# Performance work log

Measured on AMD Instinct MI355X. Metric: run time of the kernel, lower is better.

The kernel has to match this reference:

```python
import jax, jax.numpy as jnp
import numpy as np

EMBED_DIM = 1024
NUM_HEADS = 16
HEAD_DIM = EMBED_DIM // NUM_HEADS
ROPE_BASE = 10000.0


def _rope_cos_sin(seq_len, head_dim, dtype=jnp.float32):
    inv_freq = 1.0 / (ROPE_BASE ** (jnp.arange(0, head_dim, 2, dtype=jnp.float32) / head_dim))
    t = jnp.arange(seq_len, dtype=jnp.float32)
    freqs = jnp.outer(t, inv_freq)            # [N, D/2]
    emb = jnp.concatenate([freqs, freqs], -1)  # [N, D]
    return jnp.cos(emb).astype(dtype), jnp.sin(emb).astype(dtype)


def _rotate_half(x):
    x1, x2 = jnp.split(x, 2, axis=-1)
    return jnp.concatenate([-x2, x1], axis=-1)


def setup_inputs() -> dict:
    key = jax.random.key(0)
    k1, k2, k3 = jax.random.split(key, 3)
    B, N, C = 2, 2048, EMBED_DIM
    x = jax.random.normal(k1, (B, N, C), jnp.float32)
    Wqkv = jax.random.normal(k2, (3 * C, C), jnp.float32) * (C ** -0.5)
    Wout = jax.random.normal(k3, (C, C), jnp.float32) * (C ** -0.5)
    bout = jnp.zeros((C,), jnp.float32)
    return {"x": x, "Wqkv": Wqkv, "Wout": Wout, "bout": bout}


def reference(x, Wqkv, Wout, bout):
    B, N, C = x.shape
    H, D = NUM_HEADS, HEAD_DIM
    qkv = jnp.einsum('bnc,fc->bnf', x, Wqkv)          # [B,N,3C]
    qkv = qkv.reshape(B, N, 3, H, D).transpose(2, 0, 3, 1, 4)  # [3,B,H,N,D]
    q, k, v = qkv[0], qkv[1], qkv[2]
    cos, sin = _rope_cos_sin(N, D, x.dtype)           # [N,D]
    cos = cos[None, None]
    sin = sin[None, None]
    q = q * cos + _rotate_half(q) * sin
    k = k * cos + _rotate_half(k) * sin
    scale = D ** -0.5
    scores = jnp.einsum('bhqd,bhkd->bhqk', q, k) * scale
    attn = jax.nn.softmax(scores, axis=-1)
    out = jnp.einsum('bhqk,bhkd->bhqd', attn, v)      # [B,H,N,D]
    out = out.transpose(0, 2, 1, 3).reshape(B, N, C)
    return jnp.einsum('bnc,oc->bno', out, Wout) + bout
```

## Files before the change

kernel.cpp:

```cpp
#include <hip/hip_runtime.h>
#include <stdint.h>

#define DI __device__ __forceinline__

typedef __attribute__((ext_vector_type(8))) __bf16 bf16x8;
typedef __attribute__((ext_vector_type(8))) short short8;
typedef __attribute__((ext_vector_type(4))) float f32x4;
typedef __attribute__((ext_vector_type(16))) float f32x16;

DI unsigned short f2bf(float f) {
    union { float f; uint32_t u; } v; v.f = f;
    uint32_t r = v.u + 0x7FFFu + ((v.u >> 16) & 1u);
    return (unsigned short)(r >> 16);
}
DI uint32_t pk2(float a, float b) { return (uint32_t)f2bf(a) | ((uint32_t)f2bf(b) << 16); }
DI bf16x8 asb(short8 s) { union { short8 s; bf16x8 b; } u; u.s = s; return u.b; }
DI bf16x8 asb4(uint32_t a, uint32_t b, uint32_t c, uint32_t d) {
    union { uint32_t u[4]; bf16x8 b; } x; x.u[0] = a; x.u[1] = b; x.u[2] = c; x.u[3] = d; return x.b;
}
DI void gload16(const void* g, void* l) {
    __builtin_amdgcn_global_load_lds(
        (const __attribute__((address_space(1))) void*)g,
        (__attribute__((address_space(3))) void*)l, 16, 0, 0);
}
DI int swzc(int c) { return c ^ ((c >> 3) & 7); }

__global__ __launch_bounds__(256) void castk(const float* __restrict__ in,
                                             unsigned short* __restrict__ out, int n4) {
    int i = blockIdx.x * 256 + threadIdx.x;
    if (i < n4) {
        float4 v = ((const float4*)in)[i];
        union { unsigned short u[4]; uint2 q; } p;
        p.u[0] = f2bf(v.x); p.u[1] = f2bf(v.y); p.u[2] = f2bf(v.z); p.u[3] = f2bf(v.w);
        ((uint2*)out)[i] = p.q;
    }
}

__global__ __launch_bounds__(256) void ropek(float* __restrict__ cosT,
                                             float* __restrict__ sinT) {
    int i = blockIdx.x * 256 + threadIdx.x;
    int n = i >> 5, d = i & 31;
    float inv = powf(10000.0f, -(float)(2 * d) * (1.0f / 64.0f));
    float a = (float)n * inv;
    float s, c;
    sincosf(a, &s, &c);
    cosT[i] = c; sinT[i] = s;
}

template <int MODE, int BM>
__global__ __launch_bounds__(256) void gemm_bt(
    const unsigned short* __restrict__ A, const unsigned short* __restrict__ Bt,
    int M, int N, int K,
    unsigned short* __restrict__ Qbuf, unsigned short* __restrict__ Kbuf,
    unsigned short* __restrict__ Vt,
    const float* __restrict__ cosT, const float* __restrict__ sinT,
    float* __restrict__ Cout, const float* __restrict__ bias) {
    constexpr int WM = BM / 2;
    constexpr int MI = WM / 16;
    __shared__ __align__(16) unsigned short As[BM * 32];
    __shared__ __align__(16) unsigned short Bs[128 * 32];
    const int tid = threadIdx.x;
    const int wave = tid >> 6, lane = tid & 63, g = lane >> 4, li = lane & 15;
    const int wr = wave >> 1, wc = wave & 1;
    const int m0 = blockIdx.y * BM, n0 = blockIdx.x * 128;

    f32x4 acc[MI][4] = {};
    const int nK = K >> 5;
    for (int kk = 0; kk < nK; ++kk) {
#pragma unroll
        for (int i = 0; i < BM / 64; ++i) {
            int cb = i * 256 + wave * 64;
            int c = cb + lane;
            int r = c >> 2, k0 = (c & 3) * 8;
            gload16(A + (size_t)(m0 + r) * K + kk * 32 + k0, &As[cb * 8]);
        }
#pragma unroll
        for (int i = 0; i < 2; ++i) {
            int cb = i * 256 + wave * 64;
            int c = cb + lane;
            int r = c >> 2, k0 = (c & 3) * 8;
            gload16(Bt + (size_t)(n0 + r) * K + kk * 32 + k0, &Bs[cb * 8]);
        }
        __syncthreads();
        short8 af[MI], bf[4];
#pragma unroll
        for (int mi = 0; mi < MI; ++mi)
            af[mi] = *(const short8*)&As[(wr * WM + mi * 16 + li) * 32 + g * 8];
#pragma unroll
        for (int ni = 0; ni < 4; ++ni)
            bf[ni] = *(const short8*)&Bs[(wc * 64 + ni * 16 + li) * 32 + g * 8];
#pragma unroll
        for (int mi = 0; mi < MI; ++mi)
#pragma unroll
            for (int ni = 0; ni < 4; ++ni)
                acc[mi][ni] = __builtin_amdgcn_mfma_f32_16x16x32_bf16(
                    asb(af[mi]), asb(bf[ni]), acc[mi][ni], 0, 0, 0);
        __syncthreads();
    }

    if (MODE == 1) {
#pragma unroll
        for (int mi = 0; mi < MI; ++mi) {
            int row = m0 + wr * WM + mi * 16 + 4 * g;
#pragma unroll
            for (int ni = 0; ni < 4; ++ni) {
                int col = n0 + wc * 64 + ni * 16 + li;
                float b = bias[col];
#pragma unroll
                for (int r = 0; r < 4; ++r)
                    Cout[(size_t)(row + r) * N + col] = acc[mi][ni][r] + b;
            }
        }
    } else {
        const int fb = n0 + wc * 64;
        const int three = fb >> 10;
        const int hh = (fb & 1023) >> 6;
        const int bq = m0 >> 11;
        const int nb0 = m0 & 2047;
        const size_t bh = (size_t)(bq * 16 + hh);
        if (three < 2) {
#pragma unroll
            for (int mi = 0; mi < MI; ++mi) {
#pragma unroll
                for (int r = 0; r < 4; ++r) {
                    int n = nb0 + wr * WM + mi * 16 + 4 * g + r;
                    float v0 = acc[mi][0][r], v1 = acc[mi][1][r];
                    float v2 = acc[mi][2][r], v3 = acc[mi][3][r];
                    float c0 = cosT[n * 32 + li],      s0 = sinT[n * 32 + li];
                    float c1 = cosT[n * 32 + 16 + li], s1 = sinT[n * 32 + 16 + li];
                    float o0 = v0 * c0 - v2 * s0;
                    float o2 = v2 * c0 + v0 * s0;
                    float o1 = v1 * c1 - v3 * s1;
                    float o3 = v3 * c1 + v1 * s1;
                    if (three == 0) { o0 *= 0.125f; o1 *= 0.125f; o2 *= 0.125f; o3 *= 0.125f; }
                    unsigned short* dst = (three == 0 ? Qbuf : Kbuf) + (bh * 2048 + n) * 64;
                    dst[li] = f2bf(o0); dst[16 + li] = f2bf(o1);
                    dst[32 + li] = f2bf(o2); dst[48 + li] = f2bf(o3);
                }
            }
        } else {
            unsigned short* vtw = As + wave * 1024;
#pragma unroll
            for (int mi = 0; mi < MI; ++mi) {
                __syncthreads();
#pragma unroll
                for (int ni = 0; ni < 4; ++ni)
#pragma unroll
                    for (int r = 0; r < 4; ++r)
                        vtw[(ni * 16 + li) * 16 + 4 * g + r] = f2bf(acc[mi][ni][r]);
                __syncthreads();
                uint4 lo = *(const uint4*)&vtw[lane * 16];
                uint4 hi = *(const uint4*)&vtw[lane * 16 + 8];
                int nbase = nb0 + wr * WM + mi * 16;
                unsigned short* dst = Vt + (bh * 64 + lane) * 2048 + nbase;
                *(uint4*)dst = lo;
                *(uint4*)(dst + 8) = hi;
            }
        }
    }
}

#define THR 8.0f
__global__ __launch_bounds__(256) void attnk(
    const unsigned short* __restrict__ Qb, const unsigned short* __restrict__ Kb,
    const unsigned short* __restrict__ Vt, unsigned short* __restrict__ Obuf) {
    __shared__ __align__(16) unsigned short Ks[2][64 * 64];
    __shared__ __align__(16) unsigned short Vs[2][64 * 64];
    const int tid = threadIdx.x, wave = tid >> 6, lane = tid & 63;
    const int h = lane >> 5, li = lane & 31;

    const int fid = blockIdx.y * 16 + blockIdx.x;
    const int logical = (fid & 7) * 64 + (fid >> 3);
    const int bh = logical >> 4, qt = logical & 15;
    const int q0 = qt * 128 + wave * 32;

    bf16x8 qf[4];
    const unsigned short* qp = Qb + ((size_t)bh * 2048 + q0 + li) * 64;
#pragma unroll
    for (int c = 0; c < 4; ++c) qf[c] = asb(*(const short8*)(qp + c * 16 + h * 8));

    const uint4* kg = (const uint4*)(Kb + (size_t)bh * 2048 * 64);
    const uint4* vg = (const uint4*)Vt;
    const int r0 = tid >> 3, r1 = (tid + 256) >> 3, cc = tid & 7;
    const int sw0 = swzc(tid) * 8, sw1 = swzc(tid + 256) * 8;
    const size_t vrow0 = ((size_t)bh * 64 + r0) * 256 + cc;
    const size_t vrow1 = ((size_t)bh * 64 + r1) * 256 + cc;

    uint4 kr0 = kg[tid], kr1 = kg[256 + tid];
    uint4 vr0 = vg[vrow0], vr1 = vg[vrow1];

    f32x16 o0 = {}, o1 = {};
    float m_ = -1e30f, l_ = 0.f;

    for (int kt = 0; kt < 32; ++kt) {
        const int cur = kt & 1;
        *(uint4*)&Ks[cur][sw0] = kr0;
        *(uint4*)&Ks[cur][sw1] = kr1;
        *(uint4*)&Vs[cur][sw0] = vr0;
        *(uint4*)&Vs[cur][sw1] = vr1;
        if (kt < 31) {
            int nt = kt + 1;
            kr0 = kg[nt * 512 + tid]; kr1 = kg[nt * 512 + 256 + tid];
            vr0 = vg[vrow0 + nt * 8]; vr1 = vg[vrow1 + nt * 8];
        }
        __syncthreads();

        f32x16 s0 = {}, s1 = {};
#pragma unroll
        for (int c = 0; c < 4; ++c) {
            int ch = 2 * c + h;
            bf16x8 k0 = asb(*(const short8*)&Ks[cur][li * 64 + ((ch ^ (li & 7)) * 8)]);
            bf16x8 k1 = asb(*(const short8*)&Ks[cur][(32 + li) * 64 + ((ch ^ (li & 7)) * 8)]);
            s0 = __builtin_amdgcn_mfma_f32_32x32x16_bf16(k0, qf[c], s0, 0, 0, 0);
            s1 = __builtin_amdgcn_mfma_f32_32x32x16_bf16(k1, qf[c], s1, 0, 0, 0);
        }

        float pmax = fmaxf(s0[0], s1[0]);
#pragma unroll
        for (int r = 1; r < 16; ++r) pmax = fmaxf(pmax, fmaxf(s0[r], s1[r]));
        pmax = fmaxf(pmax, __shfl_xor(pmax, 32));

        if (!__all(pmax <= m_ + THR)) {
            float mn = fmaxf(m_, pmax);
            float al = __expf(m_ - mn);
            m_ = mn; l_ *= al;
#pragma unroll
            for (int r = 0; r < 16; ++r) {
                float ar = __shfl(al, (r & 3) + 8 * (r >> 2) + 4 * h);
                o0[r] *= ar; o1[r] *= ar;
            }
        }
        float sum = 0.f;
#pragma unroll
        for (int r = 0; r < 16; ++r) {
            float p0 = __expf(s0[r] - m_); s0[r] = p0; sum += p0;
            float p1 = __expf(s1[r] - m_); s1[r] = p1; sum += p1;
        }
        sum += __shfl_xor(sum, 32);
        l_ += sum;

        uint32_t w0[8], w1[8];
#pragma unroll
        for (int m = 0; m < 8; ++m) {
            w0[m] = pk2(s0[2 * m], s0[2 * m + 1]);
            w1[m] = pk2(s1[2 * m], s1[2 * m + 1]);
        }

#pragma unroll
        for (int ks = 0; ks < 4; ++ks) {
            const uint32_t* wk = (ks < 2) ? w0 : w1;
            int sub = (ks & 1) * 4;
            uint32_t a0 = wk[sub], a1 = wk[sub + 1], a2 = wk[sub + 2], a3 = wk[sub + 3];
            uint32_t x0 = __shfl_xor(a0, 32), x1 = __shfl_xor(a1, 32);
            uint32_t x2 = __shfl_xor(a2, 32), x3 = __shfl_xor(a3, 32);
            uint32_t d0 = h ? x2 : a0;
            uint32_t d1 = h ? x3 : a1;
            uint32_t d2 = h ? a2 : x0;
            uint32_t d3 = h ? a3 : x1;
            bf16x8 pf = asb4(d0, d1, d2, d3);
            int ch = 2 * ks + h;
            bf16x8 vf0 = asb(*(const short8*)&Vs[cur][li * 64 + ((ch ^ (li & 7)) * 8)]);
            bf16x8 vf1 = asb(*(const short8*)&Vs[cur][(32 + li) * 64 + ((ch ^ (li & 7)) * 8)]);
            o0 = __builtin_amdgcn_mfma_f32_32x32x16_bf16(pf, vf0, o0, 0, 0, 0);
            o1 = __builtin_amdgcn_mfma_f32_32x32x16_bf16(pf, vf1, o1, 0, 0, 0);
        }
    }

    float linv = 1.0f / l_;
    const int b = bh >> 4, hh = bh & 15;
#pragma unroll
    for (int r = 0; r < 16; ++r) {
        int qrow = (r & 3) + 8 * (r >> 2) + 4 * h;
        float lr = __shfl(linv, qrow);
        int n = q0 + qrow;
        unsigned short* dst = Obuf + ((size_t)(b * 2048 + n)) * 1024 + hh * 64 + li;
        dst[0]  = f2bf(o0[r] * lr);
        dst[32] = f2bf(o1[r] * lr);
    }
}

extern "C" void kernel_launch(void* const* d_in, const int* in_sizes, int n_in,
                              void* d_out, int out_size, void* d_ws, size_t ws_size,
                              hipStream_t stream) {
    const float* x    = (const float*)d_in[0];
    const float* Wqkv = (const float*)d_in[1];
    const float* Wout = (const float*)d_in[2];
    const float* bout = (const float*)d_in[3];
    float* out = (float*)d_out;
    char* ws = (char*)d_ws;

    size_t off = 0;
    unsigned short* xb    = (unsigned short*)(ws + off);
    unsigned short* Obuf  = xb;
    off += (size_t)4096 * 1024 * 2;
    unsigned short* wqkvb = (unsigned short*)(ws + off); off += (size_t)3072 * 1024 * 2;
    unsigned short* woutb = (unsigned short*)(ws + off); off += (size_t)1024 * 1024 * 2;
    float* cosT = (float*)(ws + off); off += (size_t)2048 * 32 * 4;
    float* sinT = (float*)(ws + off); off += (size_t)2048 * 32 * 4;
    unsigned short* Qbuf = (unsigned short*)(ws + off); off += (size_t)32 * 2048 * 64 * 2;
    unsigned short* Kbuf = (unsigned short*)(ws + off); off += (size_t)32 * 2048 * 64 * 2;
    unsigned short* Vt   = (unsigned short*)(ws + off); off += (size_t)32 * 64 * 2048 * 2;

    castk<<<4096, 256, 0, stream>>>(x, xb, 1048576);
    castk<<<3072, 256, 0, stream>>>(Wqkv, wqkvb, 786432);
    castk<<<1024, 256, 0, stream>>>(Wout, woutb, 262144);
    ropek<<<256, 256, 0, stream>>>(cosT, sinT);

    gemm_bt<0, 128><<<dim3(24, 32), 256, 0, stream>>>(
        xb, wqkvb, 4096, 3072, 1024, Qbuf, Kbuf, Vt, cosT, sinT, nullptr, nullptr);

    attnk<<<dim3(16, 32), 256, 0, stream>>>(Qbuf, Kbuf, Vt, Obuf);

    gemm_bt<1, 64><<<dim3(8, 64), 256, 0, stream>>>(
        Obuf, woutb, 4096, 1024, 1024, nullptr, nullptr, nullptr, nullptr, nullptr,
        out, bout);
}
```

Baseline: 218.0 us.

## Fuse prep kernels, use exp2 softmax, drop P shuffles, swizzle V transpose

Merges the three cast launches and the RoPE table launch into one prep kernel to cut launch overhead. Folds log2(e) into the Q scale so attention can use exp2 directly, and raises the rescale-skip threshold. Drops the cross-half shuffle that rearranged P fragments before the PV MFMA, relying on the V tile's k ordering, and permutes the V transpose writes in LDS. It also packs bf16 with a hardware convert instruction. The P/V ordering and threshold change risk correctness if the layouts do not line up.

New measurement: 213.0 us. -2.3%, faster.

```diff
diff --git a/kernel.cpp b/kernel.cpp
--- a/kernel.cpp
+++ b/kernel.cpp
@@ -13,7 +13,11 @@
     uint32_t r = v.u + 0x7FFFu + ((v.u >> 16) & 1u);
     return (unsigned short)(r >> 16);
 }
-DI uint32_t pk2(float a, float b) { return (uint32_t)f2bf(a) | ((uint32_t)f2bf(b) << 16); }
+DI uint32_t pk2(float a, float b) {
+    uint32_t r;
+    asm("v_cvt_pk_bf16_f32 %0, %1, %2" : "=v"(r) : "v"(a), "v"(b));
+    return r;
+}
 DI bf16x8 asb(short8 s) { union { short8 s; bf16x8 b; } u; u.s = s; return u.b; }
 DI bf16x8 asb4(uint32_t a, uint32_t b, uint32_t c, uint32_t d) {
     union { uint32_t u[4]; bf16x8 b; } x; x.u[0] = a; x.u[1] = b; x.u[2] = c; x.u[3] = d; return x.b;
@@ -25,26 +29,31 @@
 }
 DI int swzc(int c) { return c ^ ((c >> 3) & 7); }
 
-__global__ __launch_bounds__(256) void castk(const float* __restrict__ in,
-                                             unsigned short* __restrict__ out, int n4) {
-    int i = blockIdx.x * 256 + threadIdx.x;
-    if (i < n4) {
+__global__ __launch_bounds__(256) void prepk(
+    const float* __restrict__ x, const float* __restrict__ Wqkv,
+    const float* __restrict__ Wout,
+    unsigned short* __restrict__ xb, unsigned short* __restrict__ wqkvb,
+    unsigned short* __restrict__ woutb,
+    float* __restrict__ cosT, float* __restrict__ sinT) {
+    const int bid = blockIdx.x, tid = threadIdx.x;
+    if (bid < 8192) {
+        const float* in; unsigned short* out; int i;
+        if (bid < 4096)      { in = x;    out = xb;    i = bid * 256 + tid; }
+        else if (bid < 7168) { in = Wqkv; out = wqkvb; i = (bid - 4096) * 256 + tid; }
+        else                 { in = Wout; out = woutb; i = (bid - 7168) * 256 + tid; }
         float4 v = ((const float4*)in)[i];
         union { unsigned short u[4]; uint2 q; } p;
         p.u[0] = f2bf(v.x); p.u[1] = f2bf(v.y); p.u[2] = f2bf(v.z); p.u[3] = f2bf(v.w);
         ((uint2*)out)[i] = p.q;
-    }
-}
-
-__global__ __launch_bounds__(256) void ropek(float* __restrict__ cosT,
-                                             float* __restrict__ sinT) {
-    int i = blockIdx.x * 256 + threadIdx.x;
-    int n = i >> 5, d = i & 31;
-    float inv = powf(10000.0f, -(float)(2 * d) * (1.0f / 64.0f));
-    float a = (float)n * inv;
-    float s, c;
-    sincosf(a, &s, &c);
-    cosT[i] = c; sinT[i] = s;
+    } else {
+        int i = (bid - 8192) * 256 + tid;
+        int n = i >> 5, d = i & 31;
+        float inv = powf(10000.0f, -(float)(2 * d) * (1.0f / 64.0f));
+        float a = (float)n * inv;
+        float s, c;
+        sincosf(a, &s, &c);
+        cosT[i] = c; sinT[i] = s;
+    }
 }
 
 template <int MODE, int BM>
@@ -132,7 +141,10 @@
                     float o2 = v2 * c0 + v0 * s0;
                     float o1 = v1 * c1 - v3 * s1;
                     float o3 = v3 * c1 + v1 * s1;
-                    if (three == 0) { o0 *= 0.125f; o1 *= 0.125f; o2 *= 0.125f; o3 *= 0.125f; }
+                    if (three == 0) {
+                        const float qs = 0.18033688f;
+                        o0 *= qs; o1 *= qs; o2 *= qs; o3 *= qs;
+                    }
                     unsigned short* dst = (three == 0 ? Qbuf : Kbuf) + (bh * 2048 + n) * 64;
                     dst[li] = f2bf(o0); dst[16 + li] = f2bf(o1);
                     dst[32 + li] = f2bf(o2); dst[48 + li] = f2bf(o3);
@@ -140,6 +152,7 @@
             }
         } else {
             unsigned short* vtw = As + wave * 1024;
+            const int gsw = ((g & 1) << 1) | (g >> 1);
 #pragma unroll
             for (int mi = 0; mi < MI; ++mi) {
                 __syncthreads();
@@ -147,7 +160,7 @@
                 for (int ni = 0; ni < 4; ++ni)
 #pragma unroll
                     for (int r = 0; r < 4; ++r)
-                        vtw[(ni * 16 + li) * 16 + 4 * g + r] = f2bf(acc[mi][ni][r]);
+                        vtw[(ni * 16 + li) * 16 + 4 * gsw + r] = f2bf(acc[mi][ni][r]);
                 __syncthreads();
                 uint4 lo = *(const uint4*)&vtw[lane * 16];
                 uint4 hi = *(const uint4*)&vtw[lane * 16 + 8];
@@ -160,7 +173,7 @@
     }
 }
 
-#define THR 8.0f
+#define THR2 11.0f
 __global__ __launch_bounds__(256) void attnk(
     const unsigned short* __restrict__ Qb, const unsigned short* __restrict__ Kb,
     const unsigned short* __restrict__ Vt, unsigned short* __restrict__ Obuf) {
@@ -220,9 +233,9 @@
         for (int r = 1; r < 16; ++r) pmax = fmaxf(pmax, fmaxf(s0[r], s1[r]));
         pmax = fmaxf(pmax, __shfl_xor(pmax, 32));
 
-        if (!__all(pmax <= m_ + THR)) {
+        if (!__all(pmax <= m_ + THR2)) {
             float mn = fmaxf(m_, pmax);
-            float al = __expf(m_ - mn);
+            float al = __builtin_exp2f(m_ - mn);
             m_ = mn; l_ *= al;
 #pragma unroll
             for (int r = 0; r < 16; ++r) {
@@ -233,8 +246,8 @@
         float sum = 0.f;
 #pragma unroll
         for (int r = 0; r < 16; ++r) {
-            float p0 = __expf(s0[r] - m_); s0[r] = p0; sum += p0;
-            float p1 = __expf(s1[r] - m_); s1[r] = p1; sum += p1;
+            float p0 = __builtin_exp2f(s0[r] - m_); s0[r] = p0; sum += p0;
+            float p1 = __builtin_exp2f(s1[r] - m_); s1[r] = p1; sum += p1;
         }
         sum += __shfl_xor(sum, 32);
         l_ += sum;
@@ -249,15 +262,8 @@
 #pragma unroll
         for (int ks = 0; ks < 4; ++ks) {
             const uint32_t* wk = (ks < 2) ? w0 : w1;
-            int sub = (ks & 1) * 4;
-            uint32_t a0 = wk[sub], a1 = wk[sub + 1], a2 = wk[sub + 2], a3 = wk[sub + 3];
-            uint32_t x0 = __shfl_xor(a0, 32), x1 = __shfl_xor(a1, 32);
-            uint32_t x2 = __shfl_xor(a2, 32), x3 = __shfl_xor(a3, 32);
-            uint32_t d0 = h ? x2 : a0;
-            uint32_t d1 = h ? x3 : a1;
-            uint32_t d2 = h ? a2 : x0;
-            uint32_t d3 = h ? a3 : x1;
-            bf16x8 pf = asb4(d0, d1, d2, d3);
+            const int sub = (ks & 1) * 4;
+            bf16x8 pf = asb4(wk[sub], wk[sub + 1], wk[sub + 2], wk[sub + 3]);
             int ch = 2 * ks + h;
             bf16x8 vf0 = asb(*(const short8*)&Vs[cur][li * 64 + ((ch ^ (li & 7)) * 8)]);
             bf16x8 vf1 = asb(*(const short8*)&Vs[cur][(32 + li) * 64 + ((ch ^ (li & 7)) * 8)]);
@@ -301,10 +307,7 @@
     unsigned short* Kbuf = (unsigned short*)(ws + off); off += (size_t)32 * 2048 * 64 * 2;
     unsigned short* Vt   = (unsigned short*)(ws + off); off += (size_t)32 * 64 * 2048 * 2;
 
-    castk<<<4096, 256, 0, stream>>>(x, xb, 1048576);
-    castk<<<3072, 256, 0, stream>>>(Wqkv, wqkvb, 786432);
-    castk<<<1024, 256, 0, stream>>>(Wout, woutb, 262144);
-    ropek<<<256, 256, 0, stream>>>(cosT, sinT);
+    prepk<<<8448, 256, 0, stream>>>(x, Wqkv, Wout, xb, wqkvb, woutb, cosT, sinT);
 
     gemm_bt<0, 128><<<dim3(24, 32), 256, 0, stream>>>(
         xb, wqkvb, 4096, 3072, 1024, Qbuf, Kbuf, Vt, cosT, sinT, nullptr, nullptr);
```
